# Optimization experiments

Measured on AMD Instinct MI355X. Metric: run time of the kernel, lower is better.

## Reference

```python
import jax, jax.numpy as jnp
import numpy as np

CURVE = 1.0
TAU = 0.5
N_NODES = 32768
N_EDGES = 65536
IN_CH = 64
OUT_CH = 64
N_HEADS = 8
N_RF = 128
EPS = 1e-7


def _make_projection_matrix(m, d, seed=0):
    # FAVOR+ projection: stacked rows of transposed QR blocks, row-rescaled by chi norms.
    rng = np.random.RandomState(seed)
    blocks = []
    nb_full = m // d
    for _ in range(nb_full):
        q, _ = np.linalg.qr(rng.randn(d, d))
        blocks.append(q.T)
    rem = m - nb_full * d
    if rem > 0:
        q, _ = np.linalg.qr(rng.randn(d, d))
        blocks.append(q.T[:rem])
    final = np.vstack(blocks)  # [m, d]
    mult = np.linalg.norm(rng.randn(m, d), axis=1)
    return (mult[:, None] * final).astype(np.float32)


def _expmap0(u, c):
    # Hyperboloid exp map at origin; time slot of u is ignored.
    sqrtK = 1.0 / jnp.sqrt(c)
    x = u[..., 1:]
    xn = jnp.maximum(jnp.linalg.norm(x, axis=-1, keepdims=True), EPS)
    theta = xn / sqrtK
    return jnp.concatenate([sqrtK * jnp.cosh(theta), sqrtK * jnp.sinh(theta) * x / xn], axis=-1)


def _proj(x, c):
    # Re-project onto hyperboloid: x0 = sqrt(1/c + ||x_space||^2)
    K = 1.0 / c
    y = x[..., 1:]
    t = jnp.sqrt(K + jnp.sum(y * y, axis=-1, keepdims=True))
    return jnp.concatenate([t, y], axis=-1)


def _logmap0(x, c):
    # Hyperboloid log map at origin; output tangent has zero time component.
    sqrtK = 1.0 / jnp.sqrt(c)
    y = x[..., 1:]
    yn = jnp.maximum(jnp.linalg.norm(y, axis=-1, keepdims=True), EPS)
    t = jnp.maximum(x[..., 0:1] / sqrtK, 1.0 + EPS)
    res = sqrtK * jnp.arccosh(t) * y / yn
    return jnp.concatenate([jnp.zeros_like(res[..., :1]), res], axis=-1)


def _softmax_kernel(data, P, tau, c):
    # Performer-style exp kernel with hyperbolic (time-coordinate) prefactor.
    dt = data[..., 0:1]
    ds = data[..., 1:]
    m = 1.0 / jnp.sqrt(jnp.asarray(P.shape[0], jnp.float32))
    wx = jnp.exp(jnp.einsum('bnhd,dm->bnhm', ds, P) / jnp.sqrt(tau))
    front = jnp.exp((c / tau - dt * dt / tau) / 2.0) * m  # [b,n,h,1]
    return wx * front


def setup_inputs() -> dict:
    key = jax.random.key(0)
    k1, k2, k3, k4 = jax.random.split(key, 4)
    std = (2.0 / (IN_CH + OUT_CH)) ** 0.5
    z = 0.01 * jax.random.normal(k1, (1, N_NODES, IN_CH), jnp.float32)
    Wq = std * jax.random.normal(k2, (N_HEADS, OUT_CH, IN_CH), jnp.float32)
    Wk = std * jax.random.normal(k3, (N_HEADS, OUT_CH, IN_CH), jnp.float32)
    Wv = std * jax.random.normal(k4, (N_HEADS, OUT_CH, IN_CH), jnp.float32)
    edge_index = jax.random.randint(jax.random.fold_in(key, 7), (2, N_EDGES), 0, N_NODES, jnp.int32)
    proj_mat = jnp.asarray(_make_projection_matrix(IN_CH - 1, N_RF))  # [63, 128]
    return {"z": z, "Wq": Wq, "Wk": Wk, "Wv": Wv, "proj_mat": proj_mat, "edge_index": edge_index}


def reference(z, Wq, Wk, Wv, proj_mat, edge_index):
    c = jnp.float32(CURVE)
    tau = jnp.float32(TAU)
    zs = z[0]  # [N, C] (B == 1, squeeze)
    zh = _proj(_expmap0(zs, c), c)  # lift features to hyperboloid
    u = _logmap0(zh, c)             # [N, C], tangent at origin

    def hyplin(W):  # HypLinear (no bias): proj(expmap0(logmap0(x) @ W^T)) for all heads
        mu = jnp.einsum('nc,hoc->hno', u, W)  # [H, N, D]
        return _proj(_expmap0(mu, c), c)

    q, k, v = hyplin(Wq), hyplin(Wk), hyplin(Wv)  # [H, N, D]
    H, N, D = q.shape
    # mirrors torch stacked.reshape(-1, N, H, D) (row-major relabeling)
    query = q.reshape(1, N, H, D)
    key_ = k.reshape(1, N, H, D)
    value = v.reshape(1, N, H, D)

    qp = _softmax_kernel(query, proj_mat, tau, c).transpose(2, 0, 1, 3)  # [H,1,N,M]
    kp = _softmax_kernel(key_, proj_mat, tau, c).transpose(2, 0, 1, 3)   # [H,1,N,M]
    vv = value.transpose(2, 0, 1, 3)                                      # [H,1,N,D]

    last = jnp.einsum('hbnm,hbnd->hbmd', kp, vv)   # [H,1,M,D] kv summary
    zo = jnp.einsum('hbnm,hbmd->hbnd', qp, last)   # [H,1,N,D]
    mnorm = -zo[..., 0:1] ** 2 + jnp.sum(zo[..., 1:] ** 2, axis=-1, keepdims=True)
    zo = zo / (jnp.sqrt(c) * jnp.sqrt(jnp.abs(mnorm)))  # renormalize onto hyperboloid

    start, end = edge_index[0], edge_index[1]
    ea = jnp.einsum('hbem,hbem->hbe', qp[:, :, end, :], kp[:, :, start, :])
    A_weight = ea.transpose(1, 2, 0)  # [1, E, H]

    # hyper_agg: Euclidean head-mean followed by Minkowski renormalization
    t = jnp.mean(zo[:, 0], axis=0)  # [N, D]
    xn = -t[..., 0:1] ** 2 + jnp.sum(t[..., 1:] ** 2, axis=-1, keepdims=True)
    z_next = t / (jnp.sqrt(c) * jnp.sqrt(jnp.abs(xn)))
    link_loss = jnp.mean(A_weight)
    return z_next, link_loss
```

## Files before the change

kernel.cpp:

```cpp
#include <hip/hip_runtime.h>

#define DEV __device__ __forceinline__

#define NNODES 32768
#define NEDGES 65536
#define NROWS  262144
#define EPSF   1e-7f
#define SQRT2F 1.4142135623730951f
#define LOG2E  1.4426950408889634f
#define LOG2SQRT63 2.9886399611087573f

#define OFF_WFRAG 0u
#define OFF_LASTB 0u
#define OFF_PFRAG 196608u
#define OFF_EA    212992u
#define OFF_U     409600u
#define OFF_PART  42352640u
#define OFF_PHIQ  75907072u
#define OFF_PHIK  143015936u

typedef short s8v __attribute__((ext_vector_type(8)));
typedef float f4v __attribute__((ext_vector_type(4)));

DEV unsigned short f2bf(float f) {
  unsigned u = __float_as_uint(f);
  return (unsigned short)((u + 0x7fffu + ((u >> 16) & 1u)) >> 16);
}
DEV float bf2f(unsigned short h) { return __uint_as_float(((unsigned)h) << 16); }
DEV unsigned pack2(float lo, float hi) {
  return __builtin_amdgcn_perm(__float_as_uint(hi) + 0x8000u, __float_as_uint(lo) + 0x8000u, 0x07060302u);
}
DEV float frcp(float x) { return __builtin_amdgcn_rcpf(x); }

__global__ __launch_bounds__(256) void k01_prep(const float* __restrict__ z, unsigned short* __restrict__ ubf,
                                                const float* __restrict__ Wq, const float* __restrict__ Wk,
                                                const float* __restrict__ Wv, const float* __restrict__ P,
                                                unsigned short* __restrict__ Wfrag, unsigned short* __restrict__ Pfrag,
                                                float* __restrict__ ea) {
  int i = blockIdx.x * 256 + threadIdx.x;
  float4 v = *(const float4*)(z + (size_t)i * 4);
  if ((i & 15) == 0) v.x = 0.f;
  uint2 pk;
  pk.x = pack2(v.x, v.y);
  pk.y = pack2(v.z, v.w);
  *(uint2*)(ubf + (size_t)i * 4) = pk;

  if (blockIdx.x < 96) {
    if (i == 0) ea[0] = 0.f;
    int stride = 96 * 256;
    for (int t = i; t < 98304; t += stride) {
      int j = t & 7, lane = (t >> 3) & 63, nt = (t >> 9) & 3, ks = (t >> 11) & 1, h = (t >> 12) & 7, sm = t >> 15;
      int k = ks * 32 + (lane >> 4) * 8 + j;
      int n = nt * 16 + (lane & 15);
      const float* W = (sm == 0) ? Wq : ((sm == 1) ? Wk : Wv);
      Wfrag[t] = f2bf(W[(h * 64 + n) * 64 + k]);
    }
    for (int t = i; t < 8192; t += stride) {
      int j = t & 7, lane = (t >> 3) & 63, ks = (t >> 9) & 1, mt = (t >> 10) & 7;
      int k = ks * 32 + (lane >> 4) * 8 + j;
      int m = mt * 16 + (lane & 15);
      Pfrag[t] = (k == 0) ? (unsigned short)0 : f2bf(P[(k - 1) * 128 + m] * (SQRT2F * LOG2E));
    }
  }
}

__global__ __launch_bounds__(256) void k2_mfma(const unsigned short* __restrict__ ubf,
                                               const unsigned short* __restrict__ Wfrag,
                                               const unsigned short* __restrict__ Pfrag,
                                               unsigned short* __restrict__ phiq, unsigned short* __restrict__ phik,
                                               unsigned short* __restrict__ part) {
  __shared__ short lds_raw[18944];
  short* sbuf = lds_raw;
  float* sfront = (float*)(lds_raw + 18432);
  short* kbufT = lds_raw;
  short* vbufT = lds_raw + 8704;

  int w = threadIdx.x >> 6, lane = threadIdx.x & 63;
  int q = lane >> 4, l = lane & 15;
  int b = blockIdx.x;
  int h = b >> 8, t = b & 255;
  int n0 = t * 128 + w * 32;
  int r0 = h * 32768 + n0;

  s8v afr[2][2];
#pragma unroll
  for (int mt = 0; mt < 2; ++mt)
#pragma unroll
    for (int ks = 0; ks < 2; ++ks)
      afr[mt][ks] = *(const s8v*)(ubf + (size_t)(n0 + mt * 16 + l) * 64 + ks * 32 + q * 8);

  const s8v* Wf = (const s8v*)Wfrag;
  const s8v* Pf = (const s8v*)Pfrag;
  uint2 vkeep[2][4];

#pragma unroll
  for (int sm = 0; sm < 3; ++sm) {
    f4v acc[2][4];
#pragma unroll
    for (int mt = 0; mt < 2; ++mt)
#pragma unroll
      for (int nt = 0; nt < 4; ++nt) acc[mt][nt] = (f4v)(0.f);
#pragma unroll
    for (int ks = 0; ks < 2; ++ks)
#pragma unroll
      for (int nt = 0; nt < 4; ++nt) {
        s8v bf = Wf[(((sm * 8 + h) * 2 + ks) * 4 + nt) * 64 + lane];
#pragma unroll
        for (int mt = 0; mt < 2; ++mt)
          acc[mt][nt] = __builtin_amdgcn_mfma_f32_16x16x32_bf16(afr[mt][ks], bf, acc[mt][nt], 0, 0, 0);
      }
#pragma unroll
    for (int mt = 0; mt < 2; ++mt) {
      float rs[4];
#pragma unroll
      for (int reg = 0; reg < 4; ++reg) {
        float v0 = (l == 0) ? 0.f : acc[mt][0][reg];
        rs[reg] = v0 * v0 + acc[mt][1][reg] * acc[mt][1][reg] + acc[mt][2][reg] * acc[mt][2][reg] +
                  acc[mt][3][reg] * acc[mt][3][reg];
      }
#pragma unroll
      for (int reg = 0; reg < 4; ++reg) {
#pragma unroll
        for (int off = 1; off < 16; off <<= 1) rs[reg] += __shfl_xor(rs[reg], off, 64);
      }
      float vreg[4][4];
#pragma unroll
      for (int reg = 0; reg < 4; ++reg) {
        float x = fmaxf(sqrtf(rs[reg]), EPSF);
        float e = exp2f(x * LOG2E);
        float sh = 0.5f * (e - frcp(e));
        float ratio = sh * frcp(x);
        float sh2 = sh * sh;
        int row = mt * 16 + q * 4 + reg;
        if (sm == 2) {
          float tt2 = sqrtf(1.f + sh2);
#pragma unroll
          for (int nt = 0; nt < 4; ++nt) {
            float val = acc[mt][nt][reg] * ratio;
            if (l == 0 && nt == 0) val = tt2;
            vreg[nt][reg] = val;
          }
        } else {
          float lf = -sh2 * LOG2E - LOG2SQRT63;
          if (l == 0) sfront[(sm * 4 + w) * 32 + row] = lf;
#pragma unroll
          for (int nt = 0; nt < 4; ++nt) {
            float val = acc[mt][nt][reg] * ratio;
            if (l == 0 && nt == 0) val = 0.f;
            sbuf[(sm * 4 + w) * 2304 + row * 72 + nt * 16 + l] = (short)(__float_as_uint(val) >> 16);
          }
        }
      }
      if (sm == 2) {
#pragma unroll
        for (int nt = 0; nt < 4; ++nt) {
          vkeep[mt][nt].x = pack2(vreg[nt][0], vreg[nt][1]);
          vkeep[mt][nt].y = pack2(vreg[nt][2], vreg[nt][3]);
        }
      }
    }
  }

  uint2 keep0[8], keep1[8];
#pragma unroll
  for (int sm = 0; sm < 2; ++sm) {
    s8v bsf[2][2];
#pragma unroll
    for (int nt = 0; nt < 2; ++nt)
#pragma unroll
      for (int ks = 0; ks < 2; ++ks)
        bsf[nt][ks] = *(const s8v*)&sbuf[(sm * 4 + w) * 2304 + (nt * 16 + l) * 72 + ks * 32 + q * 8];
    float lf0 = sfront[(sm * 4 + w) * 32 + l];
    float lf1 = sfront[(sm * 4 + w) * 32 + 16 + l];
    unsigned short* dst = sm ? phik : phiq;
#pragma unroll
    for (int mt = 0; mt < 8; ++mt) {
      f4v a0 = (f4v)(0.f), a1 = (f4v)(0.f);
#pragma unroll
      for (int ks = 0; ks < 2; ++ks) {
        s8v ap = Pf[(mt * 2 + ks) * 64 + lane];
        a0 = __builtin_amdgcn_mfma_f32_16x16x32_bf16(ap, bsf[0][ks], a0, 0, 0, 0);
        a1 = __builtin_amdgcn_mfma_f32_16x16x32_bf16(ap, bsf[1][ks], a1, 0, 0, 0);
      }
      float v00 = exp2f(a0[0] + lf0), v01 = exp2f(a0[1] + lf0), v02 = exp2f(a0[2] + lf0), v03 = exp2f(a0[3] + lf0);
      float v10 = exp2f(a1[0] + lf1), v11 = exp2f(a1[1] + lf1), v12 = exp2f(a1[2] + lf1), v13 = exp2f(a1[3] + lf1);
      uint2 p0, p1;
      p0.x = pack2(v00, v01); p0.y = pack2(v02, v03);
      p1.x = pack2(v10, v11); p1.y = pack2(v12, v13);
      *(uint2*)(dst + (size_t)(r0 + l) * 128 + mt * 16 + q * 4) = p0;
      *(uint2*)(dst + (size_t)(r0 + 16 + l) * 128 + mt * 16 + q * 4) = p1;
      if (sm == 1) { keep0[mt] = p0; keep1[mt] = p1; }
    }
  }

  f4v facc[2][4];
#pragma unroll
  for (int mtl = 0; mtl < 2; ++mtl)
#pragma unroll
    for (int nt = 0; nt < 4; ++nt) facc[mtl][nt] = (f4v)(0.f);

#pragma unroll
  for (int hf = 0; hf < 2; ++hf) {
    __syncthreads();
    if ((w >> 1) == hf) {
      int nd0 = (w & 1) * 32 + l, nd1 = nd0 + 16;
#pragma unroll
      for (int mt = 0; mt < 8; ++mt) {
        int m = mt * 16 + q * 4;
        kbufT[(m + 0) * 68 + nd0] = (short)(keep0[mt].x & 0xffffu);
        kbufT[(m + 1) * 68 + nd0] = (short)(keep0[mt].x >> 16);
        kbufT[(m + 2) * 68 + nd0] = (short)(keep0[mt].y & 0xffffu);
        kbufT[(m + 3) * 68 + nd0] = (short)(keep0[mt].y >> 16);
        kbufT[(m + 0) * 68 + nd1] = (short)(keep1[mt].x & 0xffffu);
        kbufT[(m + 1) * 68 + nd1] = (short)(keep1[mt].x >> 16);
        kbufT[(m + 2) * 68 + nd1] = (short)(keep1[mt].y & 0xffffu);
        kbufT[(m + 3) * 68 + nd1] = (short)(keep1[mt].y >> 16);
      }
#pragma unroll
      for (int mt = 0; mt < 2; ++mt)
#pragma unroll
        for (int nt = 0; nt < 4; ++nt)
          *(uint2*)&vbufT[(nt * 16 + l) * 72 + (w & 1) * 32 + mt * 16 + q * 4] = vkeep[mt][nt];
    }
    __syncthreads();
#pragma unroll
    for (int kc = 0; kc < 2; ++kc) {
      s8v bv[4];
#pragma unroll
      for (int nt = 0; nt < 4; ++nt)
        bv[nt] = *(const s8v*)&vbufT[(nt * 16 + l) * 72 + kc * 32 + q * 8];
      s8v av[2];
#pragma unroll
      for (int mtl = 0; mtl < 2; ++mtl) {
        const short* kb = &kbufT[((2 * w + mtl) * 16 + l) * 68 + kc * 32 + q * 8];
        union { s8v v; long long L[2]; } ua;
        ua.L[0] = *(const long long*)kb;
        ua.L[1] = *(const long long*)(kb + 4);
        av[mtl] = ua.v;
      }
#pragma unroll
      for (int mtl = 0; mtl < 2; ++mtl)
#pragma unroll
        for (int nt = 0; nt < 4; ++nt)
          facc[mtl][nt] = __builtin_amdgcn_mfma_f32_16x16x32_bf16(av[mtl], bv[nt], facc[mtl][nt], 0, 0, 0);
    }
  }

#pragma unroll
  for (int mtl = 0; mtl < 2; ++mtl)
#pragma unroll
    for (int nt = 0; nt < 4; ++nt) {
      uint2 pk;
      pk.x = pack2(facc[mtl][nt][0], facc[mtl][nt][1]);
      pk.y = pack2(facc[mtl][nt][2], facc[mtl][nt][3]);
      int d = nt * 16 + l;
      int m = (2 * w + mtl) * 16 + q * 4;
      *(uint2*)(part + ((size_t)((t * 8 + h) * 64 + d)) * 128 + m) = pk;
    }
}

__global__ __launch_bounds__(256) void k3p_pack(const unsigned* __restrict__ part32, unsigned short* __restrict__ lastB) {
  int t2 = blockIdx.x * 256 + threadIdx.x;
  float s0 = 0.f, s1 = 0.f;
#pragma unroll 16
  for (int c = 0; c < 256; ++c) {
    unsigned v = part32[((size_t)c << 12) + t2];
    s0 += __uint_as_float(v << 16);
    s1 += __uint_as_float(v & 0xffff0000u);
  }
  int m = (t2 & 63) * 2, d = (t2 >> 6) & 63, h = t2 >> 12;
  int ks = m >> 5, j = m & 7, qq = (m >> 3) & 3;
  int lane = qq * 16 + (d & 15), nt = d >> 4;
  unsigned short* dst = &lastB[((((h * 4 + ks) * 4 + nt) * 64 + lane) << 3) + j];
  dst[0] = f2bf(s0);
  dst[1] = f2bf(s1);
}

__global__ __launch_bounds__(512) void k4_mfma(const unsigned short* __restrict__ phiq,
                                               const unsigned short* __restrict__ lastB,
                                               const float* __restrict__ ea, float* __restrict__ out) {
  __shared__ unsigned zbufT[8][64][18];
  int w = threadIdx.x >> 6, lane = threadIdx.x & 63;
  int q = lane >> 4, l = lane & 15;
  int n0 = blockIdx.x * 32;

  const s8v* Bf = (const s8v*)lastB;
  s8v bf[4][4];
#pragma unroll
  for (int ks = 0; ks < 4; ++ks)
#pragma unroll
    for (int nt = 0; nt < 4; ++nt) bf[ks][nt] = Bf[((w * 4 + ks) * 4 + nt) * 64 + lane];

  s8v af[2][4];
#pragma unroll
  for (int mt = 0; mt < 2; ++mt)
#pragma unroll
    for (int ks = 0; ks < 4; ++ks)
      af[mt][ks] = *(const s8v*)(phiq + (size_t)(8 * (n0 + mt * 16 + l) + w) * 128 + ks * 32 + q * 8);

  f4v acc[2][4];
#pragma unroll
  for (int mt = 0; mt < 2; ++mt)
#pragma unroll
    for (int nt = 0; nt < 4; ++nt) acc[mt][nt] = (f4v)(0.f);
#pragma unroll
  for (int ks = 0; ks < 4; ++ks)
#pragma unroll
    for (int nt = 0; nt < 4; ++nt)
#pragma unroll
      for (int mt = 0; mt < 2; ++mt)
        acc[mt][nt] = __builtin_amdgcn_mfma_f32_16x16x32_bf16(af[mt][ks], bf[ks][nt], acc[mt][nt], 0, 0, 0);

#pragma unroll
  for (int mt = 0; mt < 2; ++mt) {
    float rs[4];
#pragma unroll
    for (int reg = 0; reg < 4; ++reg) {
      float v0 = acc[mt][0][reg];
      float s0 = (l == 0) ? -v0 * v0 : v0 * v0;
      rs[reg] = s0 + acc[mt][1][reg] * acc[mt][1][reg] + acc[mt][2][reg] * acc[mt][2][reg] +
                acc[mt][3][reg] * acc[mt][3][reg];
    }
#pragma unroll
    for (int reg = 0; reg < 4; ++reg) {
#pragma unroll
      for (int off = 1; off < 16; off <<= 1) rs[reg] += __shfl_xor(rs[reg], off, 64);
    }
    float inv[4];
#pragma unroll
    for (int reg = 0; reg < 4; ++reg) inv[reg] = 1.f / sqrtf(fabsf(rs[reg]));
#pragma unroll
    for (int nt = 0; nt < 4; ++nt) {
      uint2 pk;
      pk.x = pack2(acc[mt][nt][0] * inv[0], acc[mt][nt][1] * inv[1]);
      pk.y = pack2(acc[mt][nt][2] * inv[2], acc[mt][nt][3] * inv[3]);
      *(uint2*)&zbufT[w][nt * 16 + l][mt * 8 + q * 2] = pk;
    }
  }
  __syncthreads();

  int tid = threadIdx.x;
  int i = tid >> 4, dg = tid & 15;
  int i2 = i >> 1, sel = i & 1;
  float s[4] = {0.f, 0.f, 0.f, 0.f};
#pragma unroll
  for (int w2 = 0; w2 < 8; ++w2) {
#pragma unroll
    for (int j = 0; j < 4; ++j) {
      unsigned u = zbufT[w2][dg * 4 + j][i2];
      s[j] += bf2f((unsigned short)(sel ? (u >> 16) : (u & 0xffffu)));
    }
  }
  float m2 = 0.f;
#pragma unroll
  for (int j = 0; j < 4; ++j) {
    s[j] *= 0.125f;
    m2 += ((dg == 0 && j == 0) ? -s[j] * s[j] : s[j] * s[j]);
  }
#pragma unroll
  for (int off = 1; off < 16; off <<= 1) m2 += __shfl_xor(m2, off, 64);
  float inv = 1.f / sqrtf(fabsf(m2));
  float4 o = make_float4(s[0] * inv, s[1] * inv, s[2] * inv, s[3] * inv);
  *(float4*)(out + (size_t)(n0 + i) * 64 + dg * 4) = o;
  if (blockIdx.x == 0 && tid == 0) out[(size_t)NNODES * 64] = ea[0] * (1.0f / 524288.0f);
}

__global__ __launch_bounds__(256) void k5_ea(const unsigned short* __restrict__ phiq,
                                             const unsigned short* __restrict__ phik,
                                             const int* __restrict__ ei, float* __restrict__ ea) {
  __shared__ float part[4];
  int lane = threadIdx.x & 63, w = threadIdx.x >> 6;
  int wid = blockIdx.x * 4 + w;
  float acc = 0.f;
  for (int i = 0; i < 16; ++i) {
    int e = wid * 16 + i;
    int s = ei[e];
    int d = ei[NEDGES + e];
    const unsigned short* bq = phiq + (size_t)d * 1024;
    const unsigned short* bk = phik + (size_t)s * 1024;
    uint4 qa = *(const uint4*)(bq + lane * 16);
    uint4 qb = *(const uint4*)(bq + lane * 16 + 8);
    uint4 ka = *(const uint4*)(bk + lane * 16);
    uint4 kb = *(const uint4*)(bk + lane * 16 + 8);
    unsigned qs[8] = {qa.x, qa.y, qa.z, qa.w, qb.x, qb.y, qb.z, qb.w};
    unsigned ks[8] = {ka.x, ka.y, ka.z, ka.w, kb.x, kb.y, kb.z, kb.w};
#pragma unroll
    for (int p = 0; p < 8; ++p) {
      float q0 = __uint_as_float(qs[p] << 16);
      float q1 = __uint_as_float(qs[p] & 0xffff0000u);
      float k0 = __uint_as_float(ks[p] << 16);
      float k1 = __uint_as_float(ks[p] & 0xffff0000u);
      acc = fmaf(q0, k0, acc);
      acc = fmaf(q1, k1, acc);
    }
  }
#pragma unroll
  for (int o = 1; o < 64; o <<= 1) acc += __shfl_xor(acc, o, 64);
  if (lane == 0) part[w] = acc;
  __syncthreads();
  if (threadIdx.x == 0) atomicAdd(ea, part[0] + part[1] + part[2] + part[3]);
}

extern "C" void kernel_launch(void* const* d_in, const int* in_sizes, int n_in,
                              void* d_out, int out_size, void* d_ws, size_t ws_size,
                              hipStream_t stream) {
  const float* z  = (const float*)d_in[0];
  const float* Wq = (const float*)d_in[1];
  const float* Wk = (const float*)d_in[2];
  const float* Wv = (const float*)d_in[3];
  const float* P  = (const float*)d_in[4];
  const int* ei   = (const int*)d_in[5];
  char* ws = (char*)d_ws;
  unsigned short* Wfrag = (unsigned short*)(ws + OFF_WFRAG);
  unsigned short* lastB = (unsigned short*)(ws + OFF_LASTB);
  unsigned short* Pfrag = (unsigned short*)(ws + OFF_PFRAG);
  float*          ea    = (float*)(ws + OFF_EA);
  unsigned short* ubf   = (unsigned short*)(ws + OFF_U);
  unsigned short* part  = (unsigned short*)(ws + OFF_PART);
  unsigned short* phiq  = (unsigned short*)(ws + OFF_PHIQ);
  unsigned short* phik  = (unsigned short*)(ws + OFF_PHIK);

  k01_prep<<<2048, 256, 0, stream>>>(z, ubf, Wq, Wk, Wv, P, Wfrag, Pfrag, ea);
  k2_mfma<<<2048, 256, 0, stream>>>(ubf, Wfrag, Pfrag, phiq, phik, part);
  k3p_pack<<<128, 256, 0, stream>>>((const unsigned*)part, lastB);
  k5_ea<<<NEDGES / 64, 256, 0, stream>>>(phiq, phik, ei, ea);
  k4_mfma<<<NNODES / 32, 512, 0, stream>>>(phiq, lastB, ea, (float*)d_out);
}
```

Measured before the change: 218.5 us.

## Store phi features and KV summary in FP8 and use FP8 MFMA

The phi_q and phi_k feature maps are now written as FP8 (e4m3) instead of bf16, and the KV summary is packed as bf8. The downstream edge-score kernel and the output MFMA kernel read these halved buffers, the latter through fp8×bf8 MFMA. The aim is to halve the memory traffic of the large phi buffers, which dominate the write in k2 and the gathers in k5 and k4. The cost is a large loss of precision in the exp-kernel features, with a risk of exceeding the output tolerance.

```diff
diff --git a/kernel.cpp b/kernel.cpp
--- a/kernel.cpp
+++ b/kernel.cpp
@@ -21,6 +21,7 @@
 
 typedef short s8v __attribute__((ext_vector_type(8)));
 typedef float f4v __attribute__((ext_vector_type(4)));
+typedef float f2v __attribute__((ext_vector_type(2)));
 
 DEV unsigned short f2bf(float f) {
   unsigned u = __float_as_uint(f);
@@ -67,7 +68,7 @@
 __global__ __launch_bounds__(256) void k2_mfma(const unsigned short* __restrict__ ubf,
                                                const unsigned short* __restrict__ Wfrag,
                                                const unsigned short* __restrict__ Pfrag,
-                                               unsigned short* __restrict__ phiq, unsigned short* __restrict__ phik,
+                                               unsigned char* __restrict__ phiq, unsigned char* __restrict__ phik,
                                                unsigned short* __restrict__ part) {
   __shared__ short lds_raw[18944];
   short* sbuf = lds_raw;
@@ -172,7 +173,7 @@
         bsf[nt][ks] = *(const s8v*)&sbuf[(sm * 4 + w) * 2304 + (nt * 16 + l) * 72 + ks * 32 + q * 8];
     float lf0 = sfront[(sm * 4 + w) * 32 + l];
     float lf1 = sfront[(sm * 4 + w) * 32 + 16 + l];
-    unsigned short* dst = sm ? phik : phiq;
+    unsigned char* dst = sm ? phik : phiq;
 #pragma unroll
     for (int mt = 0; mt < 8; ++mt) {
       f4v a0 = (f4v)(0.f), a1 = (f4v)(0.f);
@@ -184,12 +185,16 @@
       }
       float v00 = exp2f(a0[0] + lf0), v01 = exp2f(a0[1] + lf0), v02 = exp2f(a0[2] + lf0), v03 = exp2f(a0[3] + lf0);
       float v10 = exp2f(a1[0] + lf1), v11 = exp2f(a1[1] + lf1), v12 = exp2f(a1[2] + lf1), v13 = exp2f(a1[3] + lf1);
-      uint2 p0, p1;
-      p0.x = pack2(v00, v01); p0.y = pack2(v02, v03);
-      p1.x = pack2(v10, v11); p1.y = pack2(v12, v13);
-      *(uint2*)(dst + (size_t)(r0 + l) * 128 + mt * 16 + q * 4) = p0;
-      *(uint2*)(dst + (size_t)(r0 + 16 + l) * 128 + mt * 16 + q * 4) = p1;
-      if (sm == 1) { keep0[mt] = p0; keep1[mt] = p1; }
+      unsigned p0 = __builtin_amdgcn_cvt_pk_fp8_f32(v00, v01, 0, 0);
+      p0 = __builtin_amdgcn_cvt_pk_fp8_f32(v02, v03, p0, 1);
+      unsigned p1 = __builtin_amdgcn_cvt_pk_fp8_f32(v10, v11, 0, 0);
+      p1 = __builtin_amdgcn_cvt_pk_fp8_f32(v12, v13, p1, 1);
+      *(unsigned*)(dst + (size_t)(r0 + l) * 128 + mt * 16 + q * 4) = p0;
+      *(unsigned*)(dst + (size_t)(r0 + 16 + l) * 128 + mt * 16 + q * 4) = p1;
+      if (sm == 1) {
+        keep0[mt].x = pack2(v00, v01); keep0[mt].y = pack2(v02, v03);
+        keep1[mt].x = pack2(v10, v11); keep1[mt].y = pack2(v12, v13);
+      }
     }
   }
 
@@ -259,7 +264,7 @@
     }
 }
 
-__global__ __launch_bounds__(256) void k3p_pack(const unsigned* __restrict__ part32, unsigned short* __restrict__ lastB) {
+__global__ __launch_bounds__(256) void k3p_pack(const unsigned* __restrict__ part32, unsigned char* __restrict__ lastB) {
   int t2 = blockIdx.x * 256 + threadIdx.x;
   float s0 = 0.f, s1 = 0.f;
 #pragma unroll 16
@@ -271,32 +276,31 @@
   int m = (t2 & 63) * 2, d = (t2 >> 6) & 63, h = t2 >> 12;
   int ks = m >> 5, j = m & 7, qq = (m >> 3) & 3;
   int lane = qq * 16 + (d & 15), nt = d >> 4;
-  unsigned short* dst = &lastB[((((h * 4 + ks) * 4 + nt) * 64 + lane) << 3) + j];
-  dst[0] = f2bf(s0);
-  dst[1] = f2bf(s1);
-}
-
-__global__ __launch_bounds__(512) void k4_mfma(const unsigned short* __restrict__ phiq,
-                                               const unsigned short* __restrict__ lastB,
+  unsigned r = __builtin_amdgcn_cvt_pk_bf8_f32(s0, s1, 0, 0);
+  *(unsigned short*)(lastB + ((((h * 4 + ks) * 4 + nt) * 64 + lane) << 3) + j) = (unsigned short)r;
+}
+
+__global__ __launch_bounds__(512) void k4_mfma(const unsigned char* __restrict__ phiq,
+                                               const unsigned char* __restrict__ lastB,
                                                const float* __restrict__ ea, float* __restrict__ out) {
   __shared__ unsigned zbufT[8][64][18];
   int w = threadIdx.x >> 6, lane = threadIdx.x & 63;
   int q = lane >> 4, l = lane & 15;
   int n0 = blockIdx.x * 32;
 
-  const s8v* Bf = (const s8v*)lastB;
-  s8v bf[4][4];
+  const long* Bf = (const long*)lastB;
+  long bf[4][4];
 #pragma unroll
   for (int ks = 0; ks < 4; ++ks)
 #pragma unroll
     for (int nt = 0; nt < 4; ++nt) bf[ks][nt] = Bf[((w * 4 + ks) * 4 + nt) * 64 + lane];
 
-  s8v af[2][4];
+  long af[2][4];
 #pragma unroll
   for (int mt = 0; mt < 2; ++mt)
 #pragma unroll
     for (int ks = 0; ks < 4; ++ks)
-      af[mt][ks] = *(const s8v*)(phiq + (size_t)(8 * (n0 + mt * 16 + l) + w) * 128 + ks * 32 + q * 8);
+      af[mt][ks] = *(const long*)(phiq + (size_t)(8 * (n0 + mt * 16 + l) + w) * 128 + ks * 32 + q * 8);
 
   f4v acc[2][4];
 #pragma unroll
@@ -309,7 +313,7 @@
     for (int nt = 0; nt < 4; ++nt)
 #pragma unroll
       for (int mt = 0; mt < 2; ++mt)
-        acc[mt][nt] = __builtin_amdgcn_mfma_f32_16x16x32_bf16(af[mt][ks], bf[ks][nt], acc[mt][nt], 0, 0, 0);
+        acc[mt][nt] = __builtin_amdgcn_mfma_f32_16x16x32_fp8_bf8(af[mt][ks], bf[ks][nt], acc[mt][nt], 0, 0, 0);
 
 #pragma unroll
   for (int mt = 0; mt < 2; ++mt) {
@@ -365,8 +369,8 @@
   if (blockIdx.x == 0 && tid == 0) out[(size_t)NNODES * 64] = ea[0] * (1.0f / 524288.0f);
 }
 
-__global__ __launch_bounds__(256) void k5_ea(const unsigned short* __restrict__ phiq,
-                                             const unsigned short* __restrict__ phik,
+__global__ __launch_bounds__(256) void k5_ea(const unsigned char* __restrict__ phiq,
+                                             const unsigned char* __restrict__ phik,
                                              const int* __restrict__ ei, float* __restrict__ ea) {
   __shared__ float part[4];
   int lane = threadIdx.x & 63, w = threadIdx.x >> 6;
@@ -376,22 +380,20 @@
     int e = wid * 16 + i;
     int s = ei[e];
     int d = ei[NEDGES + e];
-    const unsigned short* bq = phiq + (size_t)d * 1024;
-    const unsigned short* bk = phik + (size_t)s * 1024;
-    uint4 qa = *(const uint4*)(bq + lane * 16);
-    uint4 qb = *(const uint4*)(bq + lane * 16 + 8);
-    uint4 ka = *(const uint4*)(bk + lane * 16);
-    uint4 kb = *(const uint4*)(bk + lane * 16 + 8);
-    unsigned qs[8] = {qa.x, qa.y, qa.z, qa.w, qb.x, qb.y, qb.z, qb.w};
-    unsigned ks[8] = {ka.x, ka.y, ka.z, ka.w, kb.x, kb.y, kb.z, kb.w};
-#pragma unroll
-    for (int p = 0; p < 8; ++p) {
-      float q0 = __uint_as_float(qs[p] << 16);
-      float q1 = __uint_as_float(qs[p] & 0xffff0000u);
-      float k0 = __uint_as_float(ks[p] << 16);
-      float k1 = __uint_as_float(ks[p] & 0xffff0000u);
-      acc = fmaf(q0, k0, acc);
-      acc = fmaf(q1, k1, acc);
+    uint4 qa = *(const uint4*)(phiq + (size_t)d * 1024 + lane * 16);
+    uint4 ka = *(const uint4*)(phik + (size_t)s * 1024 + lane * 16);
+    unsigned qs[4] = {qa.x, qa.y, qa.z, qa.w};
+    unsigned ks[4] = {ka.x, ka.y, ka.z, ka.w};
+#pragma unroll
+    for (int p = 0; p < 4; ++p) {
+      f2v q0 = __builtin_amdgcn_cvt_pk_f32_fp8(qs[p], 0);
+      f2v q1 = __builtin_amdgcn_cvt_pk_f32_fp8(qs[p], 1);
+      f2v k0 = __builtin_amdgcn_cvt_pk_f32_fp8(ks[p], 0);
+      f2v k1 = __builtin_amdgcn_cvt_pk_f32_fp8(ks[p], 1);
+      acc = fmaf(q0.x, k0.x, acc);
+      acc = fmaf(q0.y, k0.y, acc);
+      acc = fmaf(q1.x, k1.x, acc);
+      acc = fmaf(q1.y, k1.y, acc);
     }
   }
 #pragma unroll
@@ -412,13 +414,13 @@
   const int* ei   = (const int*)d_in[5];
   char* ws = (char*)d_ws;
   unsigned short* Wfrag = (unsigned short*)(ws + OFF_WFRAG);
-  unsigned short* lastB = (unsigned short*)(ws + OFF_LASTB);
+  unsigned char*  lastB = (unsigned char*)(ws + OFF_LASTB);
   unsigned short* Pfrag = (unsigned short*)(ws + OFF_PFRAG);
   float*          ea    = (float*)(ws + OFF_EA);
   unsigned short* ubf   = (unsigned short*)(ws + OFF_U);
   unsigned short* part  = (unsigned short*)(ws + OFF_PART);
-  unsigned short* phiq  = (unsigned short*)(ws + OFF_PHIQ);
-  unsigned short* phik  = (unsigned short*)(ws + OFF_PHIK);
+  unsigned char*  phiq  = (unsigned char*)(ws + OFF_PHIQ);
+  unsigned char*  phik  = (unsigned char*)(ws + OFF_PHIK);
 
   k01_prep<<<2048, 256, 0, stream>>>(z, ubf, Wq, Wk, Wv, P, Wfrag, Pfrag, ea);
   k2_mfma<<<2048, 256, 0, stream>>>(ubf, Wfrag, Pfrag, phiq, phik, part);
```

Measured after the change: 201.9 us. 7.6% less time.
